# Performance work log

Measured on AMD Instinct MI355X. Metric: run time of the kernel, lower is better.

Reference implementation:

```python
import jax, jax.numpy as jnp
import numpy as np

B = 2048       # batch
F_IN = 1024    # input feature dim
R_EMB = 1024   # rows of EmbedLinear sparse weight (new features)
NNZ_E = 65536  # nnz of embed sparse weight
F_OUT = 1024   # output dim of ExpandingLinear
NNZ_W = 131072 # nnz of main sparse weight [F_OUT, F_IN + R_EMB]
NNZ_B = 512    # nnz of sparse bias
F_MID = F_IN + R_EMB


def setup_inputs() -> dict:
    key = jax.random.key(0)
    ks = jax.random.split(key, 9)
    return {
        "x": jax.random.normal(ks[0], (B, F_IN), jnp.float32),
        "embed_rows": jax.random.randint(ks[1], (NNZ_E,), 0, R_EMB, jnp.int32),
        "embed_cols": jax.random.randint(ks[2], (NNZ_E,), 0, F_IN, jnp.int32),
        "embed_vals": jax.random.normal(ks[3], (NNZ_E,), jnp.float32) * 0.05,
        "w_rows": jax.random.randint(ks[4], (NNZ_W,), 0, F_OUT, jnp.int32),
        "w_cols": jax.random.randint(ks[5], (NNZ_W,), 0, F_MID, jnp.int32),
        "w_vals": jax.random.normal(ks[6], (NNZ_W,), jnp.float32) * 0.05,
        "bias_idx": jax.random.randint(ks[7], (NNZ_B,), 0, F_OUT, jnp.int32),
        "bias_vals": jax.random.normal(ks[8], (NNZ_B,), jnp.float32),
    }


def _spmm(rows, cols, vals, x, n_rows):
    # sparse COO [n_rows, F] @ x.T -> transposed: returns [B, n_rows]
    # (matches torch.sparse.mm(sparse_w, input.t()).t())
    g = vals[:, None] * x.T[cols]                              # [nnz, B] gather + scale
    return jax.ops.segment_sum(g, rows, num_segments=n_rows).T # scatter-add over rows


def reference(x, embed_rows, embed_cols, embed_vals,
              w_rows, w_cols, w_vals, bias_idx, bias_vals):
    # EmbedLinear.forward: sparse mm + ReLU + concat along features
    h = jax.nn.relu(_spmm(embed_rows, embed_cols, embed_vals, x, R_EMB))  # [B, R_EMB]
    x2 = jnp.concatenate([x, h], axis=1)                                   # [B, F_MID]
    # ExpandingLinear tail: sparse weight mm + densified sparse bias
    bias = jnp.zeros((F_OUT,), x.dtype).at[bias_idx].add(bias_vals)
    return _spmm(w_rows, w_cols, w_vals, x2, F_OUT) + bias[None, :]        # [B, F_OUT]
```

## Files before the change

kernel.cpp:

```cpp
#include <hip/hip_runtime.h>
#include <hip/hip_bf16.h>

#define B_SZ   2048
#define F_IN   1024
#define R_EMB  1024
#define F_OUT  1024
#define F_MID  2048
#define NNZ_E  65536
#define NNZ_W  131072
#define NNZ_B  512

typedef __bf16 bf16x8 __attribute__((ext_vector_type(8)));
typedef float  f32x4  __attribute__((ext_vector_type(4)));

__device__ inline void gload16(const void* g, void* l) {
    __builtin_amdgcn_global_load_lds(
        (const __attribute__((address_space(1))) void*)g,
        (__attribute__((address_space(3))) void*)l, 16, 0, 0);
}

__device__ inline ushort f2bf(float v) {
    __hip_bfloat16 h = __float2bfloat16(v);
    return *reinterpret_cast<ushort*>(&h);
}

__global__ void k_zero4(float4* __restrict__ p, int n) {
    int i = blockIdx.x * blockDim.x + threadIdx.x;
    if (i < n) p[i] = make_float4(0.f, 0.f, 0.f, 0.f);
}

__global__ void k_scatter_fused(const int* __restrict__ er, const int* __restrict__ ec,
                                const float* __restrict__ ev,
                                const int* __restrict__ wr_, const int* __restrict__ wc_,
                                const float* __restrict__ wv,
                                const int* __restrict__ bi, const float* __restrict__ bv,
                                float* __restrict__ Ef, float* __restrict__ Wf,
                                float* __restrict__ biasd) {
    int b = blockIdx.x, t = threadIdx.x;
    if (b < NNZ_E / 256) {
        int i = b * 256 + t;
        atomicAdd(&Ef[(size_t)er[i] * F_IN + ec[i]], ev[i]);
    } else if (b < NNZ_E / 256 + NNZ_W / 256) {
        int i = (b - NNZ_E / 256) * 256 + t;
        atomicAdd(&Wf[(size_t)wr_[i] * F_MID + wc_[i]], wv[i]);
    } else {
        int i = t;
        atomicAdd(&biasd[bi[i]], bv[i]);
        i += 256;
        atomicAdd(&biasd[bi[i]], bv[i]);
    }
}

__global__ void k_cvt_fused(const float4* __restrict__ x, ushort* __restrict__ x2,
                            const float4* __restrict__ Ef, ushort* __restrict__ Ebf,
                            const float4* __restrict__ Wf, ushort* __restrict__ Wbf) {
    int b = blockIdx.x, t = threadIdx.x;
    if (b < 2048) {
        int i = b * 256 + t;
        int row = i >> 8, c4 = i & 255;
        float4 v = x[i];
        ((ushort4*)x2)[(size_t)row * (F_MID / 4) + c4] =
            make_ushort4(f2bf(v.x), f2bf(v.y), f2bf(v.z), f2bf(v.w));
    } else if (b < 3072) {
        int i = (b - 2048) * 256 + t;
        float4 v = Ef[i];
        ((ushort4*)Ebf)[i] = make_ushort4(f2bf(v.x), f2bf(v.y), f2bf(v.z), f2bf(v.w));
    } else {
        int i = (b - 3072) * 256 + t;
        float4 v = Wf[i];
        ((ushort4*)Wbf)[i] = make_ushort4(f2bf(v.x), f2bf(v.y), f2bf(v.z), f2bf(v.w));
    }
}

template <int PHASE>
__global__ __launch_bounds__(256)
void k_gemm3(const ushort* __restrict__ x2,
             const ushort* __restrict__ Ebf,
             const ushort* __restrict__ Wbf,
             const float* __restrict__ biasd,
             float* __restrict__ out,
             ushort* __restrict__ hOut)
{
    constexpr int BS = 64, BK = 64, NT = 1024 / BK;
    __shared__ ushort lds[2][2][BS * BK];
    const int tid = threadIdx.x;
    const int w = tid >> 6, l = tid & 63;
    const int wr = w >> 1, wc = w & 1;
    const int la = l & 15;
    const int m0 = blockIdx.x * BS;

    int mode, ldb, n0;
    const ushort* A;
    const ushort* Bm;
    if (PHASE == 0) {
        if (blockIdx.y < 16) {
            mode = 0; A = x2;        Bm = Ebf;        ldb = F_IN;  n0 = blockIdx.y * BS;
        } else {
            mode = 1; A = x2;        Bm = Wbf;        ldb = F_MID; n0 = (blockIdx.y - 16) * BS;
        }
    } else {
        mode = 2;     A = x2 + F_IN; Bm = Wbf + F_IN; ldb = F_MID; n0 = blockIdx.y * BS;
    }

    const int srow = w * 8 + (l >> 3);
    const int ldst = w * 512 + l * 8;

    f32x4 acc[2][2] = {};

    #define STAGE(buf, k0)                                                        \
        _Pragma("unroll")                                                         \
        for (int i = 0; i < 2; ++i) {                                             \
            int row = i * 32 + srow;                                              \
            int scol = (k0) + ((((l & 7) ^ (row & 7))) << 3);                     \
            gload16(A  + (size_t)(m0 + row) * F_MID + scol,                       \
                    &lds[buf][0][i * 2048 + ldst]);                               \
            gload16(Bm + (size_t)(n0 + row) * ldb + scol,                         \
                    &lds[buf][1][i * 2048 + ldst]);                               \
        }

    STAGE(0, 0);
    __syncthreads();

    for (int t = 0; t < NT; ++t) {
        const int cur = t & 1;
        if (t + 1 < NT) STAGE(cur ^ 1, (t + 1) * BK);

        const ushort* sA = &lds[cur][0][0];
        const ushort* sB = &lds[cur][1][0];
        #pragma unroll
        for (int ks = 0; ks < 2; ++ks) {
            const int k8 = ks * 4 + (l >> 4);
            bf16x8 af[2], bg[2];
            #pragma unroll
            for (int m = 0; m < 2; ++m) {
                int row = wr * 32 + m * 16 + la;
                af[m] = *(const bf16x8*)(sA + row * BK + ((k8 ^ (row & 7)) << 3));
            }
            #pragma unroll
            for (int n = 0; n < 2; ++n) {
                int row = wc * 32 + n * 16 + la;
                bg[n] = *(const bf16x8*)(sB + row * BK + ((k8 ^ (row & 7)) << 3));
            }
            #pragma unroll
            for (int m = 0; m < 2; ++m)
                #pragma unroll
                for (int n = 0; n < 2; ++n)
                    acc[m][n] = __builtin_amdgcn_mfma_f32_16x16x32_bf16(
                        af[m], bg[n], acc[m][n], 0, 0, 0);
        }
        __syncthreads();
    }
    #undef STAGE

    const int lr = (l >> 4) * 4;
    #pragma unroll
    for (int m = 0; m < 2; ++m) {
        #pragma unroll
        for (int n = 0; n < 2; ++n) {
            const int col = n0 + wc * 32 + n * 16 + la;
            if (mode == 0) {
                #pragma unroll
                for (int j = 0; j < 4; ++j) {
                    int row = m0 + wr * 32 + m * 16 + lr + j;
                    hOut[(size_t)row * F_MID + col] = f2bf(fmaxf(acc[m][n][j], 0.f));
                }
            } else if (mode == 1) {
                const float bv = biasd[col];
                #pragma unroll
                for (int j = 0; j < 4; ++j) {
                    int row = m0 + wr * 32 + m * 16 + lr + j;
                    out[(size_t)row * F_OUT + col] = acc[m][n][j] + bv;
                }
            } else {
                #pragma unroll
                for (int j = 0; j < 4; ++j) {
                    int row = m0 + wr * 32 + m * 16 + lr + j;
                    out[(size_t)row * F_OUT + col] += acc[m][n][j];
                }
            }
        }
    }
}

extern "C" void kernel_launch(void* const* d_in, const int* in_sizes, int n_in,
                              void* d_out, int out_size, void* d_ws, size_t ws_size,
                              hipStream_t stream) {
    const float* x          = (const float*)d_in[0];
    const int*   embed_rows = (const int*)  d_in[1];
    const int*   embed_cols = (const int*)  d_in[2];
    const float* embed_vals = (const float*)d_in[3];
    const int*   w_rows     = (const int*)  d_in[4];
    const int*   w_cols     = (const int*)  d_in[5];
    const float* w_vals     = (const float*)d_in[6];
    const int*   bias_idx   = (const int*)  d_in[7];
    const float* bias_vals  = (const float*)d_in[8];
    float* out = (float*)d_out;

    char* ws = (char*)d_ws;
    ushort* x2    = (ushort*)ws;
    float*  Wf    = (float*)(ws + (8u << 20));
    float*  Ef    = (float*)(ws + (16u << 20));
    float*  biasd = (float*)(ws + (20u << 20));
    ushort* Ebf   = (ushort*)(ws + (20u << 20) + 4096);
    ushort* Wbf   = (ushort*)(ws + (22u << 20) + 4096);

    k_zero4<<<3073, 256, 0, stream>>>((float4*)(ws + (8u << 20)), 786688);

    k_scatter_fused<<<NNZ_E / 256 + NNZ_W / 256 + 1, 256, 0, stream>>>(
        embed_rows, embed_cols, embed_vals,
        w_rows, w_cols, w_vals,
        bias_idx, bias_vals, Ef, Wf, biasd);

    k_cvt_fused<<<5120, 256, 0, stream>>>((const float4*)x, x2,
                                          (const float4*)Ef, Ebf,
                                          (const float4*)Wf, Wbf);

    k_gemm3<0><<<dim3(B_SZ / 64, 32), 256, 0, stream>>>(
        x2, Ebf, Wbf, biasd, out, x2 + F_IN);

    k_gemm3<1><<<dim3(B_SZ / 64, 16), 256, 0, stream>>>(
        x2, Ebf, Wbf, biasd, out, x2 + F_IN);
}
```

Before: 55.36 us.

## Share A-tile between embed and weight GEMMs and swizzle block order

```diff
diff --git a/kernel.cpp b/kernel.cpp
--- a/kernel.cpp
+++ b/kernel.cpp
@@ -72,50 +72,134 @@
     }
 }
 
-template <int PHASE>
 __global__ __launch_bounds__(256)
-void k_gemm3(const ushort* __restrict__ x2,
+void k_gemmA(const ushort* __restrict__ x2,
              const ushort* __restrict__ Ebf,
              const ushort* __restrict__ Wbf,
              const float* __restrict__ biasd,
              float* __restrict__ out,
              ushort* __restrict__ hOut)
 {
-    constexpr int BS = 64, BK = 64, NT = 1024 / BK;
-    __shared__ ushort lds[2][2][BS * BK];
+    constexpr int BK = 64, NT = 16;
+    __shared__ ushort lds[2][3][64 * 64];
     const int tid = threadIdx.x;
     const int w = tid >> 6, l = tid & 63;
     const int wr = w >> 1, wc = w & 1;
     const int la = l & 15;
-    const int m0 = blockIdx.x * BS;
-
-    int mode, ldb, n0;
-    const ushort* A;
-    const ushort* Bm;
-    if (PHASE == 0) {
-        if (blockIdx.y < 16) {
-            mode = 0; A = x2;        Bm = Ebf;        ldb = F_IN;  n0 = blockIdx.y * BS;
-        } else {
-            mode = 1; A = x2;        Bm = Wbf;        ldb = F_MID; n0 = (blockIdx.y - 16) * BS;
-        }
-    } else {
-        mode = 2;     A = x2 + F_IN; Bm = Wbf + F_IN; ldb = F_MID; n0 = blockIdx.y * BS;
-    }
+
+    const int blk = blockIdx.x;
+    const int sw  = (blk & 7) * 64 + (blk >> 3);
+    const int m0  = (sw >> 4) * 64;
+    const int n0  = (sw & 15) * 64;
 
     const int srow = w * 8 + (l >> 3);
     const int ldst = w * 512 + l * 8;
 
+    f32x4 accE[2][2] = {}, accW[2][2] = {};
+
+    #define STAGE(buf, k0)                                                      \
+        _Pragma("unroll")                                                       \
+        for (int i = 0; i < 2; ++i) {                                           \
+            int row = i * 32 + srow;                                            \
+            int scol = (k0) + ((((l & 7) ^ (row & 7))) << 3);                   \
+            gload16(x2  + (size_t)(m0 + row) * F_MID + scol,                    \
+                    &lds[buf][0][i * 2048 + ldst]);                             \
+            gload16(Ebf + (size_t)(n0 + row) * F_IN + scol,                     \
+                    &lds[buf][1][i * 2048 + ldst]);                             \
+            gload16(Wbf + (size_t)(n0 + row) * F_MID + scol,                    \
+                    &lds[buf][2][i * 2048 + ldst]);                             \
+        }
+
+    STAGE(0, 0);
+    __syncthreads();
+
+    for (int t = 0; t < NT; ++t) {
+        const int cur = t & 1;
+        if (t + 1 < NT) STAGE(cur ^ 1, (t + 1) * BK);
+
+        const ushort* sA  = &lds[cur][0][0];
+        const ushort* sBE = &lds[cur][1][0];
+        const ushort* sBW = &lds[cur][2][0];
+        #pragma unroll
+        for (int ks = 0; ks < 2; ++ks) {
+            const int k8 = ks * 4 + (l >> 4);
+            bf16x8 af[2], be[2], bw[2];
+            #pragma unroll
+            for (int m = 0; m < 2; ++m) {
+                int row = wr * 32 + m * 16 + la;
+                af[m] = *(const bf16x8*)(sA + row * BK + ((k8 ^ (row & 7)) << 3));
+            }
+            #pragma unroll
+            for (int n = 0; n < 2; ++n) {
+                int row = wc * 32 + n * 16 + la;
+                be[n] = *(const bf16x8*)(sBE + row * BK + ((k8 ^ (row & 7)) << 3));
+                bw[n] = *(const bf16x8*)(sBW + row * BK + ((k8 ^ (row & 7)) << 3));
+            }
+            #pragma unroll
+            for (int m = 0; m < 2; ++m)
+                #pragma unroll
+                for (int n = 0; n < 2; ++n) {
+                    accE[m][n] = __builtin_amdgcn_mfma_f32_16x16x32_bf16(
+                        af[m], be[n], accE[m][n], 0, 0, 0);
+                    accW[m][n] = __builtin_amdgcn_mfma_f32_16x16x32_bf16(
+                        af[m], bw[n], accW[m][n], 0, 0, 0);
+                }
+        }
+        __syncthreads();
+    }
+    #undef STAGE
+
+    const int lr = (l >> 4) * 4;
+    #pragma unroll
+    for (int m = 0; m < 2; ++m) {
+        #pragma unroll
+        for (int n = 0; n < 2; ++n) {
+            const int col = n0 + wc * 32 + n * 16 + la;
+            const float bv = biasd[col];
+            #pragma unroll
+            for (int j = 0; j < 4; ++j) {
+                const int row = m0 + wr * 32 + m * 16 + lr + j;
+                hOut[(size_t)row * F_MID + col] = f2bf(fmaxf(accE[m][n][j], 0.f));
+                out[(size_t)row * F_OUT + col]  = accW[m][n][j] + bv;
+            }
+        }
+    }
+}
+
+__global__ __launch_bounds__(256)
+void k_gemmB(const ushort* __restrict__ x2,
+             const ushort* __restrict__ Wbf,
+             float* __restrict__ out)
+{
+    constexpr int BK = 64, NT = 16;
+    __shared__ ushort lds[2][2][64 * 64];
+    const int tid = threadIdx.x;
+    const int w = tid >> 6, l = tid & 63;
+    const int wr = w >> 1, wc = w & 1;
+    const int la = l & 15;
+
+    const int blk = blockIdx.x;
+    const int sw  = (blk & 7) * 64 + (blk >> 3);
+    const int m0  = (sw >> 4) * 64;
+    const int n0  = (sw & 15) * 64;
+
+    const ushort* A  = x2 + F_IN;
+    const ushort* Bm = Wbf + F_IN;
+
+    const int srow = w * 8 + (l >> 3);
+    const int ldst = w * 512 + l * 8;
+
     f32x4 acc[2][2] = {};
 
-    #define STAGE(buf, k0)                                                        \
-        _Pragma("unroll")                                                         \
-        for (int i = 0; i < 2; ++i) {                                             \
-            int row = i * 32 + srow;                                              \
-            int scol = (k0) + ((((l & 7) ^ (row & 7))) << 3);                     \
-            gload16(A  + (size_t)(m0 + row) * F_MID + scol,                       \
-                    &lds[buf][0][i * 2048 + ldst]);                               \
-            gload16(Bm + (size_t)(n0 + row) * ldb + scol,                         \
-                    &lds[buf][1][i * 2048 + ldst]);                               \
+    #define STAGE(buf, k0)                                                      \
+        _Pragma("unroll")                                                       \
+        for (int i = 0; i < 2; ++i) {                                           \
+            int row = i * 32 + srow;                                            \
+            int scol = (k0) + ((((l & 7) ^ (row & 7))) << 3);                   \
+            gload16(A  + (size_t)(m0 + row) * F_MID + scol,                     \
+                    &lds[buf][0][i * 2048 + ldst]);                             \
+            gload16(Bm + (size_t)(n0 + row) * F_MID + scol,                     \
+                    &lds[buf][1][i * 2048 + ldst]);                             \
         }
 
     STAGE(0, 0);
@@ -158,25 +242,10 @@
         #pragma unroll
         for (int n = 0; n < 2; ++n) {
             const int col = n0 + wc * 32 + n * 16 + la;
-            if (mode == 0) {
-                #pragma unroll
-                for (int j = 0; j < 4; ++j) {
-                    int row = m0 + wr * 32 + m * 16 + lr + j;
-                    hOut[(size_t)row * F_MID + col] = f2bf(fmaxf(acc[m][n][j], 0.f));
-                }
-            } else if (mode == 1) {
-                const float bv = biasd[col];
-                #pragma unroll
-                for (int j = 0; j < 4; ++j) {
-                    int row = m0 + wr * 32 + m * 16 + lr + j;
-                    out[(size_t)row * F_OUT + col] = acc[m][n][j] + bv;
-                }
-            } else {
-                #pragma unroll
-                for (int j = 0; j < 4; ++j) {
-                    int row = m0 + wr * 32 + m * 16 + lr + j;
-                    out[(size_t)row * F_OUT + col] += acc[m][n][j];
-                }
+            #pragma unroll
+            for (int j = 0; j < 4; ++j) {
+                const int row = m0 + wr * 32 + m * 16 + lr + j;
+                out[(size_t)row * F_OUT + col] += acc[m][n][j];
             }
         }
     }
@@ -215,9 +284,7 @@
                                           (const float4*)Ef, Ebf,
                                           (const float4*)Wf, Wbf);
 
-    k_gemm3<0><<<dim3(B_SZ / 64, 32), 256, 0, stream>>>(
-        x2, Ebf, Wbf, biasd, out, x2 + F_IN);
-
-    k_gemm3<1><<<dim3(B_SZ / 64, 16), 256, 0, stream>>>(
-        x2, Ebf, Wbf, biasd, out, x2 + F_IN);
-}
+    k_gemmA<<<512, 256, 0, stream>>>(x2, Ebf, Wbf, biasd, out, x2 + F_IN);
+
+    k_gemmB<<<512, 256, 0, stream>>>(x2, Wbf, out);
+}
```

Result: no change. 55.01 us (-0.6%).

## Scatter sparse weights directly into bf16 via CAS and restructure GEMM phases

Applied to the files above, without the earlier changes.

```diff
diff --git a/kernel.cpp b/kernel.cpp
--- a/kernel.cpp
+++ b/kernel.cpp
@@ -24,98 +24,99 @@
     return *reinterpret_cast<ushort*>(&h);
 }
 
-__global__ void k_zero4(float4* __restrict__ p, int n) {
-    int i = blockIdx.x * blockDim.x + threadIdx.x;
-    if (i < n) p[i] = make_float4(0.f, 0.f, 0.f, 0.f);
-}
-
-__global__ void k_scatter_fused(const int* __restrict__ er, const int* __restrict__ ec,
-                                const float* __restrict__ ev,
-                                const int* __restrict__ wr_, const int* __restrict__ wc_,
-                                const float* __restrict__ wv,
-                                const int* __restrict__ bi, const float* __restrict__ bv,
-                                float* __restrict__ Ef, float* __restrict__ Wf,
-                                float* __restrict__ biasd) {
+__device__ inline float bf2f(ushort u) {
+    uint w = (uint)u << 16;
+    float f;
+    __builtin_memcpy(&f, &w, 4);
+    return f;
+}
+
+__device__ inline void bf16_scatter_add(ushort* addr, float val) {
+    uint* word = (uint*)((uintptr_t)addr & ~(uintptr_t)3);
+    const bool hi = ((uintptr_t)addr & 2) != 0;
+    uint old = __hip_atomic_load(word, __ATOMIC_RELAXED, __HIP_MEMORY_SCOPE_AGENT);
+    while (true) {
+        ushort cur = hi ? (ushort)(old >> 16) : (ushort)(old & 0xffffu);
+        ushort nv  = f2bf(bf2f(cur) + val);
+        uint neww  = hi ? ((old & 0x0000ffffu) | ((uint)nv << 16))
+                        : ((old & 0xffff0000u) | (uint)nv);
+        uint prev = atomicCAS(word, old, neww);
+        if (prev == old) break;
+        old = prev;
+    }
+}
+
+__global__ void k_zerocvt(float4* __restrict__ zbase,
+                          const float4* __restrict__ x, ushort* __restrict__ x2) {
     int b = blockIdx.x, t = threadIdx.x;
-    if (b < NNZ_E / 256) {
+    if (b < 1537) {
         int i = b * 256 + t;
-        atomicAdd(&Ef[(size_t)er[i] * F_IN + ec[i]], ev[i]);
-    } else if (b < NNZ_E / 256 + NNZ_W / 256) {
-        int i = (b - NNZ_E / 256) * 256 + t;
-        atomicAdd(&Wf[(size_t)wr_[i] * F_MID + wc_[i]], wv[i]);
+        if (i < 393472) zbase[i] = make_float4(0.f, 0.f, 0.f, 0.f);
     } else {
-        int i = t;
-        atomicAdd(&biasd[bi[i]], bv[i]);
-        i += 256;
-        atomicAdd(&biasd[bi[i]], bv[i]);
-    }
-}
-
-__global__ void k_cvt_fused(const float4* __restrict__ x, ushort* __restrict__ x2,
-                            const float4* __restrict__ Ef, ushort* __restrict__ Ebf,
-                            const float4* __restrict__ Wf, ushort* __restrict__ Wbf) {
-    int b = blockIdx.x, t = threadIdx.x;
-    if (b < 2048) {
-        int i = b * 256 + t;
+        int i = (b - 1537) * 256 + t;
         int row = i >> 8, c4 = i & 255;
         float4 v = x[i];
         ((ushort4*)x2)[(size_t)row * (F_MID / 4) + c4] =
             make_ushort4(f2bf(v.x), f2bf(v.y), f2bf(v.z), f2bf(v.w));
-    } else if (b < 3072) {
-        int i = (b - 2048) * 256 + t;
-        float4 v = Ef[i];
-        ((ushort4*)Ebf)[i] = make_ushort4(f2bf(v.x), f2bf(v.y), f2bf(v.z), f2bf(v.w));
+    }
+}
+
+__global__ void k_scatter(const int* __restrict__ er, const int* __restrict__ ec,
+                          const float* __restrict__ ev,
+                          const int* __restrict__ wr_, const int* __restrict__ wc_,
+                          const float* __restrict__ wv,
+                          const int* __restrict__ bi, const float* __restrict__ bv,
+                          ushort* __restrict__ Ebf, ushort* __restrict__ Wbf,
+                          float* __restrict__ biasd) {
+    int b = blockIdx.x, t = threadIdx.x;
+    if (b < NNZ_E / 256) {
+        int i = b * 256 + t;
+        bf16_scatter_add(&Ebf[(size_t)er[i] * F_IN + ec[i]], ev[i]);
+    } else if (b < NNZ_E / 256 + NNZ_W / 256) {
+        int i = (b - NNZ_E / 256) * 256 + t;
+        bf16_scatter_add(&Wbf[(size_t)wr_[i] * F_MID + wc_[i]], wv[i]);
     } else {
-        int i = (b - 3072) * 256 + t;
-        float4 v = Wf[i];
-        ((ushort4*)Wbf)[i] = make_ushort4(f2bf(v.x), f2bf(v.y), f2bf(v.z), f2bf(v.w));
-    }
-}
-
-template <int PHASE>
+        int i = (b - NNZ_E / 256 - NNZ_W / 256) * 256 + t;
+        if (i < NNZ_B) atomicAdd(&biasd[bi[i]], bv[i]);
+    }
+}
+
+template <int MODE>
 __global__ __launch_bounds__(256)
-void k_gemm3(const ushort* __restrict__ x2,
-             const ushort* __restrict__ Ebf,
-             const ushort* __restrict__ Wbf,
-             const float* __restrict__ biasd,
-             float* __restrict__ out,
-             ushort* __restrict__ hOut)
+void k_gemm(const ushort* __restrict__ x2,
+            const ushort* __restrict__ Bmat,
+            const float* __restrict__ biasd,
+            float* __restrict__ out,
+            ushort* __restrict__ hOut)
 {
-    constexpr int BS = 64, BK = 64, NT = 1024 / BK;
-    __shared__ ushort lds[2][2][BS * BK];
+    constexpr int BK = 64;
+    constexpr int NT  = (MODE == 0) ? 16 : 32;
+    constexpr int LDB = (MODE == 0) ? F_IN : F_MID;
+    __shared__ ushort lds[2][2][64 * 64];
     const int tid = threadIdx.x;
     const int w = tid >> 6, l = tid & 63;
     const int wr = w >> 1, wc = w & 1;
     const int la = l & 15;
-    const int m0 = blockIdx.x * BS;
-
-    int mode, ldb, n0;
-    const ushort* A;
-    const ushort* Bm;
-    if (PHASE == 0) {
-        if (blockIdx.y < 16) {
-            mode = 0; A = x2;        Bm = Ebf;        ldb = F_IN;  n0 = blockIdx.y * BS;
-        } else {
-            mode = 1; A = x2;        Bm = Wbf;        ldb = F_MID; n0 = (blockIdx.y - 16) * BS;
-        }
-    } else {
-        mode = 2;     A = x2 + F_IN; Bm = Wbf + F_IN; ldb = F_MID; n0 = blockIdx.y * BS;
-    }
+
+    const int blk = blockIdx.x;
+    const int sw  = (blk & 7) * 64 + (blk >> 3);
+    const int m0  = (sw >> 4) * 64;
+    const int n0  = (sw & 15) * 64;
 
     const int srow = w * 8 + (l >> 3);
     const int ldst = w * 512 + l * 8;
 
     f32x4 acc[2][2] = {};
 
-    #define STAGE(buf, k0)                                                        \
-        _Pragma("unroll")                                                         \
-        for (int i = 0; i < 2; ++i) {                                             \
-            int row = i * 32 + srow;                                              \
-            int scol = (k0) + ((((l & 7) ^ (row & 7))) << 3);                     \
-            gload16(A  + (size_t)(m0 + row) * F_MID + scol,                       \
-                    &lds[buf][0][i * 2048 + ldst]);                               \
-            gload16(Bm + (size_t)(n0 + row) * ldb + scol,                         \
-                    &lds[buf][1][i * 2048 + ldst]);                               \
+    #define STAGE(buf, k0)                                                      \
+        _Pragma("unroll")                                                       \
+        for (int i = 0; i < 2; ++i) {                                           \
+            int row = i * 32 + srow;                                            \
+            int scol = (k0) + ((((l & 7) ^ (row & 7))) << 3);                   \
+            gload16(x2   + (size_t)(m0 + row) * F_MID + scol,                   \
+                    &lds[buf][0][i * 2048 + ldst]);                             \
+            gload16(Bmat + (size_t)(n0 + row) * LDB + scol,                     \
+                    &lds[buf][1][i * 2048 + ldst]);                             \
         }
 
     STAGE(0, 0);
@@ -158,24 +159,18 @@
         #pragma unroll
         for (int n = 0; n < 2; ++n) {
             const int col = n0 + wc * 32 + n * 16 + la;
-            if (mode == 0) {
+            if (MODE == 0) {
                 #pragma unroll
                 for (int j = 0; j < 4; ++j) {
                     int row = m0 + wr * 32 + m * 16 + lr + j;
                     hOut[(size_t)row * F_MID + col] = f2bf(fmaxf(acc[m][n][j], 0.f));
                 }
-            } else if (mode == 1) {
+            } else {
                 const float bv = biasd[col];
                 #pragma unroll
                 for (int j = 0; j < 4; ++j) {
                     int row = m0 + wr * 32 + m * 16 + lr + j;
                     out[(size_t)row * F_OUT + col] = acc[m][n][j] + bv;
-                }
-            } else {
-                #pragma unroll
-                for (int j = 0; j < 4; ++j) {
-                    int row = m0 + wr * 32 + m * 16 + lr + j;
-                    out[(size_t)row * F_OUT + col] += acc[m][n][j];
                 }
             }
         }
@@ -198,26 +193,19 @@
 
     char* ws = (char*)d_ws;
     ushort* x2    = (ushort*)ws;
-    float*  Wf    = (float*)(ws + (8u << 20));
-    float*  Ef    = (float*)(ws + (16u << 20));
     float*  biasd = (float*)(ws + (20u << 20));
     ushort* Ebf   = (ushort*)(ws + (20u << 20) + 4096);
     ushort* Wbf   = (ushort*)(ws + (22u << 20) + 4096);
 
-    k_zero4<<<3073, 256, 0, stream>>>((float4*)(ws + (8u << 20)), 786688);
-
-    k_scatter_fused<<<NNZ_E / 256 + NNZ_W / 256 + 1, 256, 0, stream>>>(
+    k_zerocvt<<<1537 + 2048, 256, 0, stream>>>((float4*)biasd,
+                                               (const float4*)x, x2);
+
+    k_scatter<<<NNZ_E / 256 + NNZ_W / 256 + (NNZ_B + 255) / 256, 256, 0, stream>>>(
         embed_rows, embed_cols, embed_vals,
         w_rows, w_cols, w_vals,
-        bias_idx, bias_vals, Ef, Wf, biasd);
-
-    k_cvt_fused<<<5120, 256, 0, stream>>>((const float4*)x, x2,
-                                          (const float4*)Ef, Ebf,
-                                          (const float4*)Wf, Wbf);
-
-    k_gemm3<0><<<dim3(B_SZ / 64, 32), 256, 0, stream>>>(
-        x2, Ebf, Wbf, biasd, out, x2 + F_IN);
-
-    k_gemm3<1><<<dim3(B_SZ / 64, 16), 256, 0, stream>>>(
-        x2, Ebf, Wbf, biasd, out, x2 + F_IN);
-}
+        bias_idx, bias_vals, Ebf, Wbf, biasd);
+
+    k_gemm<0><<<512, 256, 0, stream>>>(x2, Ebf, biasd, out, x2 + F_IN);
+
+    k_gemm<1><<<512, 256, 0, stream>>>(x2, Wbf, biasd, out, x2 + F_IN);
+}
```

Result: slower. 64.46 us (+16.5%).
